# Optimization experiments

Hardware: AMD Instinct MI355X
Metric: run time of the kernel (lower is better)

The kernel has to match this reference:

```python
import jax, jax.numpy as jnp
import numpy as np

B, S, DIM = 2, 2048, 2048
H = 16
Q_RANK, KV_RANK = 512, 512
D_NOPE, D_ROPE, D_V = 128, 64, 128
D_QK = D_NOPE + D_ROPE  # 192
EPS = 1e-6
SCALE = D_QK ** -0.5


def setup_inputs() -> dict:
    key = jax.random.key(0)
    ks = jax.random.split(key, 8)
    x = jax.random.normal(ks[0], (B, S, DIM), dtype=jnp.float32)
    # real RoPE table: theta_i = 10000^{-2i/d}, angles = pos * theta
    inv_freq = 1.0 / (10000.0 ** (np.arange(0, D_ROPE, 2, dtype=np.float32) / D_ROPE))
    ang = np.arange(S, dtype=np.float32)[:, None] * inv_freq[None, :]  # (S, D_ROPE//2)
    freqs_cis = jnp.asarray(np.stack([np.cos(ang), np.sin(ang)], axis=-1))  # (S, 32, 2)
    std = 0.02
    wq_a = jax.random.normal(ks[1], (Q_RANK, DIM), dtype=jnp.float32) * std
    wq_b = jax.random.normal(ks[2], (H * D_QK, Q_RANK), dtype=jnp.float32) * std
    wkv_a = jax.random.normal(ks[3], (KV_RANK + D_ROPE, DIM), dtype=jnp.float32) * std
    wkv_b = jax.random.normal(ks[4], (H * (D_NOPE + D_V), KV_RANK), dtype=jnp.float32) * std
    wo = jax.random.normal(ks[5], (DIM, H * D_V), dtype=jnp.float32) * std
    q_norm_w = jnp.ones((Q_RANK,), dtype=jnp.float32)
    kv_norm_w = jnp.ones((KV_RANK,), dtype=jnp.float32)
    return {"x": x, "freqs_cis": freqs_cis, "wq_a": wq_a, "wq_b": wq_b,
            "q_norm_w": q_norm_w, "wkv_a": wkv_a, "kv_norm_w": kv_norm_w,
            "wkv_b": wkv_b, "wo": wo}


def _rmsnorm(x, w):
    var = jnp.mean(jnp.square(x), axis=-1, keepdims=True)
    return x * jax.lax.rsqrt(var + EPS) * w


def _rope(x, freqs_cis):
    # x: (B, S, h, d); freqs_cis: (S, d//2, 2) as (cos, sin). Pairs are interleaved (x0,x1),(x2,x3),...
    xr, xi = x[..., 0::2], x[..., 1::2]
    cos = freqs_cis[None, :, None, :, 0]
    sin = freqs_cis[None, :, None, :, 1]
    yr = xr * cos - xi * sin
    yi = xr * sin + xi * cos
    return jnp.stack([yr, yi], axis=-1).reshape(x.shape)


def reference(x, freqs_cis, wq_a, wq_b, q_norm_w, wkv_a, kv_norm_w, wkv_b, wo):
    b, s, _ = x.shape
    # low-rank Q projection: wq_a -> RMSNorm -> wq_b
    q = _rmsnorm(x @ wq_a.T, q_norm_w) @ wq_b.T
    q = q.reshape(b, s, H, D_QK)
    q_nope, q_pe = q[..., :D_NOPE], q[..., D_NOPE:]
    q = jnp.concatenate([q_nope, _rope(q_pe, freqs_cis)], axis=-1)  # (b,s,H,192)
    # KV path
    kv = x @ wkv_a.T  # (b,s,KV_RANK+D_ROPE)
    kv_lat, k_pe = kv[..., :KV_RANK], kv[..., KV_RANK:]
    k_pe = _rope(k_pe[:, :, None, :], freqs_cis)  # (b,s,1,64)
    kv = (_rmsnorm(kv_lat, kv_norm_w) @ wkv_b.T).reshape(b, s, H, D_NOPE + D_V)
    k_nope, v = kv[..., :D_NOPE], kv[..., D_NOPE:]
    k = jnp.concatenate([k_nope, jnp.broadcast_to(k_pe, (b, s, H, D_ROPE))], axis=-1)
    # causal scaled-dot-product attention
    scores = jnp.einsum('bshd,bthd->bhst', q, k) * SCALE
    mask = jnp.tril(jnp.ones((s, s), dtype=bool))
    scores = jnp.where(mask[None, None], scores, jnp.finfo(scores.dtype).min)
    probs = jax.nn.softmax(scores, axis=-1)
    out = jnp.einsum('bhst,bthd->bshd', probs, v).reshape(b, s, H * D_V)
    return out @ wo.T
```

## Files before the change

### kernel.cpp

```cpp
#include <hip/hip_runtime.h>
#include <cstdint>
#include <cstddef>


typedef unsigned short u16;
typedef unsigned int u32;
typedef unsigned long long u64;
typedef __attribute__((ext_vector_type(8))) short bf16x8;
typedef __attribute__((ext_vector_type(4))) float floatx4;

#define MFMA16x16x32 __builtin_amdgcn_mfma_f32_16x16x32_bf16

#define QSCALE 0.10411755f
#define THR_L2 11.541560f

__device__ __forceinline__ u16 f2bf(float f) {
  u32 u = __float_as_uint(f);
  u32 r = (u + 0x7fffu + ((u >> 16) & 1u)) >> 16;
  return (u16)r;
}
__device__ __forceinline__ float bf2f(u16 b) {
  return __uint_as_float(((u32)b) << 16);
}
__device__ __forceinline__ u32 cvtpk(float lo, float hi) {
  u32 r;
  asm("v_cvt_pk_bf16_f32 %0, %1, %2" : "=v"(r) : "v"(lo), "v"(hi));
  return r;
}
__device__ __forceinline__ void gload16(const void* g, void* l) {
  __builtin_amdgcn_global_load_lds(
      (const __attribute__((address_space(1))) void*)g,
      (__attribute__((address_space(3))) void*)l, 16, 0, 0);
}

__global__ __launch_bounds__(256) void cvt_all(
    const float* __restrict__ s0, const float* __restrict__ s1,
    const float* __restrict__ s2, const float* __restrict__ s3,
    const float* __restrict__ s4, const float* __restrict__ s5,
    u16* __restrict__ d0, u16* __restrict__ d1, u16* __restrict__ d2,
    u16* __restrict__ d3, u16* __restrict__ d4, u16* __restrict__ d5) {
  constexpr int ST1 = 2097152;
  constexpr int ST2 = ST1 + 262144;
  constexpr int ST3 = ST2 + 294912;
  constexpr int ST4 = ST3 + 393216;
  constexpr int ST5 = ST4 + 524288;
  constexpr int TOT = ST5 + 1048576;
  int i = blockIdx.x * 256 + threadIdx.x;
  int stride = gridDim.x * 256;
  for (; i < TOT; i += stride) {
    const float* sp;
    u16* dp;
    int j;
    if (i < ST1)      { sp = s0; dp = d0; j = i; }
    else if (i < ST2) { sp = s1; dp = d1; j = i - ST1; }
    else if (i < ST3) { sp = s2; dp = d2; j = i - ST2; }
    else if (i < ST4) { sp = s3; dp = d3; j = i - ST3; }
    else if (i < ST5) { sp = s4; dp = d4; j = i - ST4; }
    else              { sp = s5; dp = d5; j = i - ST5; }
    float4 v = ((const float4*)sp)[j];
    ushort4 o;
    o.x = f2bf(v.x); o.y = f2bf(v.y); o.z = f2bf(v.z); o.w = f2bf(v.w);
    ((ushort4*)dp)[j] = o;
  }
}

template <int BM, int BN, int EPI>
__global__ __launch_bounds__(512) void gemm8(const u16* __restrict__ A,
                                             const u16* __restrict__ B,
                                             void* __restrict__ Cv,
                                             int M, int N, int K,
                                             const float* __restrict__ fcp,
                                             void* __restrict__ aux) {
  constexpr int WM = BM / 2;
  constexpr int AF = WM / 16;
  constexpr int WN = BN / 4;
  constexpr int FN = WN / 16;
  constexpr int LA = BM * 4 / 512;
  constexpr int LB = BN * 4 / 512;
  constexpr int S = LA + LB;
  __shared__ alignas(16) u16 As[2][BM * 32];
  __shared__ alignas(16) u16 Bs[2][BN * 32];
  const int m0 = blockIdx.y * BM, n0 = blockIdx.x * BN;
  const int t = threadIdx.x;
  const int wv = t >> 6, lane = t & 63, g = lane >> 4, qq = lane & 15;
  const int wr = wv >> 2, wc = wv & 3;
  const int fsw = (qq >> 1) & 3;
  size_t aoff[LA], boff[LB];
#pragma unroll
  for (int i = 0; i < LA; ++i) {
    int seg = t + i * 512;
    int row = seg >> 2, sl = seg & 3;
    aoff[i] = (size_t)(m0 + row) * K + (sl ^ ((row >> 1) & 3)) * 8;
  }
#pragma unroll
  for (int i = 0; i < LB; ++i) {
    int seg = t + i * 512;
    int row = seg >> 2, sl = seg & 3;
    boff[i] = (size_t)(n0 + row) * K + (sl ^ ((row >> 1) & 3)) * 8;
  }
  const floatx4 fz = {0.f, 0.f, 0.f, 0.f};
  floatx4 acc[AF][FN];
#pragma unroll
  for (int m = 0; m < AF; ++m)
#pragma unroll
    for (int n = 0; n < FN; ++n) acc[m][n] = fz;

#define GS8(buf, k0)                                                          \
  {                                                                           \
    _Pragma("unroll") for (int i = 0; i < LA; ++i)                            \
        gload16(&A[aoff[i] + (k0)], &As[buf][(size_t)(wv * 64 + i * 512) * 8]); \
    _Pragma("unroll") for (int i = 0; i < LB; ++i)                            \
        gload16(&B[boff[i] + (k0)], &Bs[buf][(size_t)(wv * 64 + i * 512) * 8]); \
  }

  const int nk = K >> 5;
  GS8(0, 0);
  GS8(1, 32);
  for (int kt = 0; kt < nk; ++kt) {
    asm volatile("" ::: "memory");
    if (kt + 1 < nk) {
      if constexpr (S == 4)
        asm volatile("s_waitcnt vmcnt(4)" ::: "memory");
      else if constexpr (S == 3)
        asm volatile("s_waitcnt vmcnt(3)" ::: "memory");
      else
        asm volatile("s_waitcnt vmcnt(2)" ::: "memory");
    } else {
      asm volatile("s_waitcnt vmcnt(0)" ::: "memory");
    }
    __builtin_amdgcn_s_barrier();
    asm volatile("" ::: "memory");
    const u16* Ab = &As[kt & 1][0];
    const u16* Bb = &Bs[kt & 1][0];
    bf16x8 af[AF], bfr[FN];
#pragma unroll
    for (int m = 0; m < AF; ++m)
      af[m] = *(const bf16x8*)&Ab[(wr * WM + m * 16 + qq) * 32 + ((g ^ fsw) * 8)];
#pragma unroll
    for (int n = 0; n < FN; ++n)
      bfr[n] = *(const bf16x8*)&Bb[(wc * WN + n * 16 + qq) * 32 + ((g ^ fsw) * 8)];
    asm volatile("s_waitcnt lgkmcnt(0)" ::: "memory");
    __builtin_amdgcn_s_barrier();
    asm volatile("" ::: "memory");
    if (kt + 2 < nk) GS8(kt & 1, (kt + 2) * 32);
    __builtin_amdgcn_s_setprio(1);
#pragma unroll
    for (int m = 0; m < AF; ++m)
#pragma unroll
      for (int n = 0; n < FN; ++n)
        acc[m][n] = MFMA16x16x32(af[m], bfr[n], acc[m][n], 0, 0, 0);
    __builtin_amdgcn_s_setprio(0);
  }
#undef GS8

#pragma unroll
  for (int m = 0; m < AF; ++m)
#pragma unroll
    for (int n = 0; n < FN; ++n) {
      const int col16 = n0 + wc * WN + n * 16;
      if constexpr (EPI == 0 || EPI == 1) {
#pragma unroll
        for (int r = 0; r < 4; ++r) {
          int row = m0 + wr * WM + m * 16 + 4 * g + r;
          int col = col16 + qq;
          if constexpr (EPI == 1)
            ((u16*)Cv)[(size_t)row * N + col] = f2bf(acc[m][n][r]);
          else
            ((float*)Cv)[(size_t)row * N + col] = acc[m][n][r];
        }
      } else if constexpr (EPI == 2) {
        const int h = col16 / 192;
        const int jb = col16 - h * 192 + qq;
#pragma unroll
        for (int r = 0; r < 4; ++r) {
          int row = m0 + wr * WM + m * 16 + 4 * g + r;
          int b = row >> 11, s = row & 2047;
          float own = acc[m][n][r];
          float par = __shfl_xor(own, 1);
          if ((qq & 1) == 0) {
            u32 w;
            if (jb < 128) {
              w = cvtpk(own * QSCALE, par * QSCALE);
            } else {
              int jp = (jb - 128) >> 1;
              float c = fcp[(s * 32 + jp) * 2];
              float sn = fcp[(s * 32 + jp) * 2 + 1];
              w = cvtpk((own * c - par * sn) * QSCALE,
                        (own * sn + par * c) * QSCALE);
            }
            *(u32*)((u16*)Cv + ((size_t)(b * 16 + h) * 2048 + s) * 192 + jb) = w;
          }
        }
      } else {
        const int h = col16 >> 8;
        const int jb = (col16 & 255) + qq;
        if (jb < 128) {
#pragma unroll
          for (int r = 0; r < 4; ++r) {
            int row = m0 + wr * WM + m * 16 + 4 * g + r;
            int b = row >> 11, s = row & 2047;
            float own = acc[m][n][r];
            float par = __shfl_xor(own, 1);
            if ((qq & 1) == 0)
              *(u32*)((u16*)Cv + ((size_t)(b * 16 + h) * 2048 + s) * 192 + jb) =
                  cvtpk(own, par);
          }
        } else {
          int row0 = m0 + wr * WM + m * 16 + 4 * g;
          int b = row0 >> 11, s0v = row0 & 2047;
          int dv = jb - 128;
          u32 lo = cvtpk(acc[m][n][0], acc[m][n][1]);
          u32 hi = cvtpk(acc[m][n][2], acc[m][n][3]);
          u64 w = (u64)lo | ((u64)hi << 32);
          *(u64*)((u16*)aux + ((size_t)(b * 16 + h) * 128 + dv) * 2048 + s0v) = w;
        }
      }
    }
}

__global__ __launch_bounds__(256) void rmsnorm_u16(const u16* __restrict__ in,
                                                   int stride,
                                                   const float* __restrict__ w,
                                                   u16* __restrict__ out) {
  const int row = blockIdx.x, t = threadIdx.x;
  __shared__ float wsum[4];
  u32 wv2 = *(const u32*)&in[(size_t)row * stride + 2 * t];
  float vx = bf2f((u16)wv2), vy = bf2f((u16)(wv2 >> 16));
  float ss = vx * vx + vy * vy;
#pragma unroll
  for (int off = 1; off < 64; off <<= 1) ss += __shfl_xor(ss, off);
  if ((t & 63) == 0) wsum[t >> 6] = ss;
  __syncthreads();
  float tot = wsum[0] + wsum[1] + wsum[2] + wsum[3];
  float r = rsqrtf(tot * (1.f / 512.f) + 1e-6f);
  *(u32*)&out[(size_t)row * 512 + 2 * t] =
      cvtpk(vx * r * w[2 * t], vy * r * w[2 * t + 1]);
}

__global__ __launch_bounds__(256) void rope_kpe_bcast(const u16* __restrict__ ap,
                                                      const float* __restrict__ fc,
                                                      u16* __restrict__ kbf) {
  int idx = blockIdx.x * 256 + threadIdx.x;
  int row = idx >> 5, j = idx & 31;
  int b = row >> 11, s = row & 2047;
  u32 wv2 = *(const u32*)&ap[(size_t)row * 1280 + 1024 + 2 * j];
  float xr = bf2f((u16)wv2), xi = bf2f((u16)(wv2 >> 16));
  float c = fc[(s * 32 + j) * 2], sn = fc[(s * 32 + j) * 2 + 1];
  u32 w = cvtpk(xr * c - xi * sn, xr * sn + xi * c);
#pragma unroll
  for (int h = 0; h < 16; ++h)
    *(u32*)&kbf[((size_t)(b * 16 + h) * 2048 + s) * 192 + 128 + 2 * j] = w;
}

__global__ __launch_bounds__(256, 4) void flash_attn(const u16* __restrict__ Q,
                                                     const u16* __restrict__ Kc,
                                                     const u16* __restrict__ VT,
                                                     u16* __restrict__ O) {
  __shared__ alignas(16) u16 Ks[2][32 * 192];
  __shared__ alignas(16) u16 Vs[2][128 * 32];
  const int QT[32] = {31, 30, 29, 28, 27, 26, 25, 24, 0,  1,  2,  3,  4,  5,
                      6,  7,  23, 22, 21, 20, 19, 18, 17, 16, 8,  9,  10, 11,
                      12, 13, 14, 15};
  const int bid = blockIdx.x;
  const int qt = QT[bid >> 5];
  const int bh = bid & 31;
  const int t = threadIdx.x, wv = t >> 6, lane = t & 63;
  const int g = lane >> 4, qq = lane & 15;
  const int qrow0 = qt * 64 + wv * 16;
  const int my_last = qrow0 + 15;
  const int q_glob = qrow0 + qq;
  const int nkt = 2 * qt + 2;

  int koffg[3], voffg[2];
#pragma unroll
  for (int i = 0; i < 3; ++i) {
    int seg = t + i * 256;
    int row = seg / 24, sl = seg - row * 24;
    koffg[i] = row * 192 + (sl ^ ((row >> 1) & 7)) * 8;
  }
#pragma unroll
  for (int i = 0; i < 2; ++i) {
    int seg = t + i * 256;
    int row = seg >> 2, sl = seg & 3;
    voffg[i] = row * 2048 + (sl ^ ((row >> 1) & 3)) * 8;
  }
  const u16* Kt0 = Kc + (size_t)bh * 2048 * 192;
  const u16* Vt0 = VT + (size_t)bh * 128 * 2048;

  bf16x8 qf[6];
  {
    const u16* qp = Q + ((size_t)bh * 2048 + qrow0 + qq) * 192;
#pragma unroll
    for (int kk = 0; kk < 6; ++kk) qf[kk] = *(const bf16x8*)&qp[kk * 32 + g * 8];
  }
  asm volatile("s_waitcnt vmcnt(0)" ::: "memory");

  const floatx4 fz = {0.f, 0.f, 0.f, 0.f};
  floatx4 oacc[8];
  floatx4 oacc_l = fz;
#pragma unroll
  for (int d = 0; d < 8; ++d) oacc[d] = fz;
  float m_run = -1e30f;

  bf16x8 ones;
#pragma unroll
  for (int i = 0; i < 8; ++i) ones[i] = (short)0x3f80;

  const int krow0 = 2 * qq;
  const int krow1 = 2 * qq + 1;
  const int xrk = qq & 7;
  const int vsw = (qq >> 1) & 3;

#define STAGE(buf, kt)                                                       \
  {                                                                          \
    const u16* Kg = Kt0 + (size_t)(kt) * (32 * 192);                         \
    const u16* Vg = Vt0 + (kt) * 32;                                         \
    _Pragma("unroll") for (int i = 0; i < 3; ++i)                            \
        gload16(Kg + koffg[i], &Ks[buf][(size_t)(wv * 64 + i * 256) * 8]);   \
    _Pragma("unroll") for (int i = 0; i < 2; ++i)                            \
        gload16(Vg + voffg[i], &Vs[buf][(size_t)(wv * 64 + i * 256) * 8]);   \
  }

  STAGE(0, 0);
  for (int kt = 0; kt < nkt; ++kt) {
    const int k0 = kt * 32;
    asm volatile("" ::: "memory");
    if (kt + 1 < nkt) {
      STAGE((kt + 1) & 1, kt + 1);
      asm volatile("s_waitcnt vmcnt(5)" ::: "memory");
    } else {
      asm volatile("s_waitcnt vmcnt(0)" ::: "memory");
    }
    __builtin_amdgcn_s_barrier();
    asm volatile("" ::: "memory");
    if (k0 <= my_last) {
      const u16* Kb = &Ks[kt & 1][0];
      const u16* Vb = &Vs[kt & 1][0];
      floatx4 s0 = fz, s1 = fz;
      __builtin_amdgcn_s_setprio(1);
#pragma unroll
      for (int kk = 0; kk < 6; ++kk) {
        int sl = kk * 4 + g;
        bf16x8 a0 = *(const bf16x8*)&Kb[krow0 * 192 + ((sl ^ xrk) * 8)];
        bf16x8 a1 = *(const bf16x8*)&Kb[krow1 * 192 + ((sl ^ xrk) * 8)];
        s0 = MFMA16x16x32(a0, qf[kk], s0, 0, 0, 0);
        s1 = MFMA16x16x32(a1, qf[kk], s1, 0, 0, 0);
      }
      __builtin_amdgcn_s_setprio(0);
      float v[8];
      if (k0 + 31 <= qrow0) {
#pragma unroll
        for (int r = 0; r < 4; ++r) {
          v[r] = s0[r];
          v[4 + r] = s1[r];
        }
      } else {
#pragma unroll
        for (int r = 0; r < 4; ++r) {
          int key0 = k0 + 8 * g + 2 * r;
          v[r] = (key0 <= q_glob) ? s0[r] : -1e30f;
          v[4 + r] = (key0 + 1 <= q_glob) ? s1[r] : -1e30f;
        }
      }
      float mloc = fmaxf(fmaxf(fmaxf(v[0], v[1]), fmaxf(v[2], v[3])),
                         fmaxf(fmaxf(v[4], v[5]), fmaxf(v[6], v[7])));
      if (!__all(mloc <= m_run + THR_L2)) {
        float mx = fmaxf(mloc, __shfl_xor(mloc, 16));
        mx = fmaxf(mx, __shfl_xor(mx, 32));
        float m_new = fmaxf(m_run, mx);
        float alpha = exp2f(m_run - m_new);
        m_run = m_new;
#pragma unroll
        for (int d = 0; d < 8; ++d)
#pragma unroll
          for (int r = 0; r < 4; ++r) oacc[d][r] *= alpha;
#pragma unroll
        for (int r = 0; r < 4; ++r) oacc_l[r] *= alpha;
      }
      float pex[8];
#pragma unroll
      for (int i = 0; i < 8; ++i) pex[i] = exp2f(v[i] - m_run);
      bf16x8 pf;
      ((u32*)&pf)[0] = cvtpk(pex[0], pex[4]);
      ((u32*)&pf)[1] = cvtpk(pex[1], pex[5]);
      ((u32*)&pf)[2] = cvtpk(pex[2], pex[6]);
      ((u32*)&pf)[3] = cvtpk(pex[3], pex[7]);
      __builtin_amdgcn_s_setprio(1);
#pragma unroll
      for (int d = 0; d < 8; ++d) {
        bf16x8 vf = *(const bf16x8*)&Vb[(d * 16 + qq) * 32 + ((g ^ vsw) * 8)];
        oacc[d] = MFMA16x16x32(vf, pf, oacc[d], 0, 0, 0);
      }
      oacc_l = MFMA16x16x32(ones, pf, oacc_l, 0, 0, 0);
      __builtin_amdgcn_s_setprio(0);
    }
    asm volatile("" ::: "memory");
    __builtin_amdgcn_s_barrier();
  }
#undef STAGE
  float linv = 1.f / oacc_l[0];
  const int b = bh >> 4, h = bh & 15;
  size_t rowoff = ((size_t)b * 2048 + qrow0 + qq) * 2048 + h * 128 + 4 * g;
#pragma unroll
  for (int d = 0; d < 8; ++d) {
    u32 lo = cvtpk(oacc[d][0] * linv, oacc[d][1] * linv);
    u32 hi = cvtpk(oacc[d][2] * linv, oacc[d][3] * linv);
    u64 w = (u64)lo | ((u64)hi << 32);
    *(u64*)&O[rowoff + d * 16] = w;
  }
}

extern "C" void kernel_launch(void* const* d_in, const int* in_sizes, int n_in,
                              void* d_out, int out_size, void* d_ws,
                              size_t ws_size, hipStream_t stream) {
  (void)in_sizes; (void)n_in; (void)out_size;
  const float* x = (const float*)d_in[0];
  const float* fc = (const float*)d_in[1];
  const float* wqa = (const float*)d_in[2];
  const float* wqb = (const float*)d_in[3];
  const float* qnw = (const float*)d_in[4];
  const float* wkva = (const float*)d_in[5];
  const float* kvnw = (const float*)d_in[6];
  const float* wkvb = (const float*)d_in[7];
  const float* wo = (const float*)d_in[8];
  float* out = (float*)d_out;
  char* ws = (char*)d_ws;

  size_t off = 0;
  auto alloc = [&](size_t bytes) {
    size_t o = off;
    off += (bytes + 255) & ~(size_t)255;
    return o;
  };
  const size_t o_xbf = alloc(16777216);
  const size_t o_wa = alloc(5242880);
  const size_t o_wqb = alloc(3145728);
  const size_t o_wkvb = alloc(4194304);
  const size_t o_wo = alloc(8388608);
  const size_t o_qln = alloc(4194304);
  const size_t o_kvln = alloc(4194304);
  const size_t o_ap = alloc(10485760);
  const size_t o_qbf = alloc(25165824);
  const size_t o_kbf = alloc(25165824);
  const size_t o_vt = alloc(16777216);
  if (ws_size < off) return;

  u16* xbf = (u16*)(ws + o_xbf);
  u16* wab = (u16*)(ws + o_wa);
  u16* wqbb = (u16*)(ws + o_wqb);
  u16* wkvbb = (u16*)(ws + o_wkvb);
  u16* wob = (u16*)(ws + o_wo);
  u16* qlatn = (u16*)(ws + o_qln);
  u16* kvlatn = (u16*)(ws + o_kvln);
  u16* ap = (u16*)(ws + o_ap);
  u16* qbf = (u16*)(ws + o_qbf);
  u16* kbf = (u16*)(ws + o_kbf);
  u16* vt = (u16*)(ws + o_vt);
  u16* attnbf = (u16*)(ws + o_xbf);

  cvt_all<<<2048, 256, 0, stream>>>(x, wqa, wkva, wqb, wkvb, wo,
                                    xbf, wab, wab + 1048576, wqbb, wkvbb, wob);

  gemm8<128, 128, 1><<<dim3(10, 32), 512, 0, stream>>>(
      xbf, wab, ap, 4096, 1280, 2048, nullptr, nullptr);
  rmsnorm_u16<<<4096, 256, 0, stream>>>(ap, 1280, qnw, qlatn);
  rmsnorm_u16<<<4096, 256, 0, stream>>>(ap + 512, 1280, kvnw, kvlatn);
  rope_kpe_bcast<<<512, 256, 0, stream>>>(ap, fc, kbf);

  gemm8<128, 256, 2><<<dim3(12, 32), 512, 0, stream>>>(
      qlatn, wqbb, qbf, 4096, 3072, 512, fc, nullptr);

  gemm8<128, 256, 3><<<dim3(16, 32), 512, 0, stream>>>(
      kvlatn, wkvbb, kbf, 4096, 4096, 512, nullptr, vt);

  flash_attn<<<1024, 256, 0, stream>>>(qbf, kbf, vt, attnbf);
  gemm8<128, 128, 0><<<dim3(16, 32), 512, 0, stream>>>(
      attnbf, wob, out, 4096, 2048, 2048, nullptr, nullptr);
}
```

Before: 248.5 us.

## Use 128-row query tiles with 8 waves in flash attention and fuse RMSNorm launches

Flash attention now uses 512-thread blocks covering 128 query rows, so each K/V tile staged into shared memory serves twice as many waves. The grid is halved and the staging and wait counts are rearranged to match. This cuts redundant global K/V traffic, at the cost of coarser causal load balance and fewer blocks in flight. The two RMSNorm launches are also merged into one kernel to save a launch.

```diff
diff --git a/kernel.cpp b/kernel.cpp
--- a/kernel.cpp
+++ b/kernel.cpp
@@ -218,13 +218,19 @@
     }
 }
 
-__global__ __launch_bounds__(256) void rmsnorm_u16(const u16* __restrict__ in,
-                                                   int stride,
-                                                   const float* __restrict__ w,
-                                                   u16* __restrict__ out) {
-  const int row = blockIdx.x, t = threadIdx.x;
+__global__ __launch_bounds__(256) void rmsnorm2(const u16* __restrict__ ap,
+                                                const float* __restrict__ qw,
+                                                const float* __restrict__ kw,
+                                                u16* __restrict__ qout,
+                                                u16* __restrict__ kout) {
+  const int bid = blockIdx.x, t = threadIdx.x;
+  const bool isq = bid < 4096;
+  const int row = isq ? bid : bid - 4096;
+  const u16* in = ap + (size_t)row * 1280 + (isq ? 0 : 512);
+  const float* w = isq ? qw : kw;
+  u16* out = (isq ? qout : kout) + (size_t)row * 512;
   __shared__ float wsum[4];
-  u32 wv2 = *(const u32*)&in[(size_t)row * stride + 2 * t];
+  u32 wv2 = *(const u32*)&in[2 * t];
   float vx = bf2f((u16)wv2), vy = bf2f((u16)(wv2 >> 16));
   float ss = vx * vx + vy * vy;
 #pragma unroll
@@ -233,8 +239,7 @@
   __syncthreads();
   float tot = wsum[0] + wsum[1] + wsum[2] + wsum[3];
   float r = rsqrtf(tot * (1.f / 512.f) + 1e-6f);
-  *(u32*)&out[(size_t)row * 512 + 2 * t] =
-      cvtpk(vx * r * w[2 * t], vy * r * w[2 * t + 1]);
+  *(u32*)&out[2 * t] = cvtpk(vx * r * w[2 * t], vy * r * w[2 * t + 1]);
 }
 
 __global__ __launch_bounds__(256) void rope_kpe_bcast(const u16* __restrict__ ap,
@@ -252,37 +257,32 @@
     *(u32*)&kbf[((size_t)(b * 16 + h) * 2048 + s) * 192 + 128 + 2 * j] = w;
 }
 
-__global__ __launch_bounds__(256, 4) void flash_attn(const u16* __restrict__ Q,
+__global__ __launch_bounds__(512, 4) void flash_attn(const u16* __restrict__ Q,
                                                      const u16* __restrict__ Kc,
                                                      const u16* __restrict__ VT,
                                                      u16* __restrict__ O) {
   __shared__ alignas(16) u16 Ks[2][32 * 192];
   __shared__ alignas(16) u16 Vs[2][128 * 32];
-  const int QT[32] = {31, 30, 29, 28, 27, 26, 25, 24, 0,  1,  2,  3,  4,  5,
-                      6,  7,  23, 22, 21, 20, 19, 18, 17, 16, 8,  9,  10, 11,
-                      12, 13, 14, 15};
+  const int QT16[16] = {15, 14, 13, 12, 11, 10, 9, 8, 0, 1, 2, 3, 4, 5, 6, 7};
   const int bid = blockIdx.x;
-  const int qt = QT[bid >> 5];
+  const int qt = QT16[bid >> 5];
   const int bh = bid & 31;
   const int t = threadIdx.x, wv = t >> 6, lane = t & 63;
   const int g = lane >> 4, qq = lane & 15;
-  const int qrow0 = qt * 64 + wv * 16;
+  const int qrow0 = qt * 128 + wv * 16;
   const int my_last = qrow0 + 15;
   const int q_glob = qrow0 + qq;
-  const int nkt = 2 * qt + 2;
-
-  int koffg[3], voffg[2];
-#pragma unroll
-  for (int i = 0; i < 3; ++i) {
-    int seg = t + i * 256;
-    int row = seg / 24, sl = seg - row * 24;
-    koffg[i] = row * 192 + (sl ^ ((row >> 1) & 7)) * 8;
-  }
-#pragma unroll
-  for (int i = 0; i < 2; ++i) {
-    int seg = t + i * 256;
-    int row = seg >> 2, sl = seg & 3;
-    voffg[i] = row * 2048 + (sl ^ ((row >> 1) & 3)) * 8;
+  const int nkt = 4 * qt + 4;
+
+  int koffg0, koffg1, voffg0;
+  {
+    int row = t / 24, sl = t - row * 24;
+    koffg0 = row * 192 + (sl ^ ((row >> 1) & 7)) * 8;
+    int seg = t + 512;
+    row = seg / 24; sl = seg - row * 24;
+    koffg1 = row * 192 + (sl ^ ((row >> 1) & 7)) * 8;
+    row = t >> 2; sl = t & 3;
+    voffg0 = row * 2048 + (sl ^ ((row >> 1) & 3)) * 8;
   }
   const u16* Kt0 = Kc + (size_t)bh * 2048 * 192;
   const u16* Vt0 = VT + (size_t)bh * 128 * 2048;
@@ -311,14 +311,13 @@
   const int xrk = qq & 7;
   const int vsw = (qq >> 1) & 3;
 
-#define STAGE(buf, kt)                                                       \
-  {                                                                          \
-    const u16* Kg = Kt0 + (size_t)(kt) * (32 * 192);                         \
-    const u16* Vg = Vt0 + (kt) * 32;                                         \
-    _Pragma("unroll") for (int i = 0; i < 3; ++i)                            \
-        gload16(Kg + koffg[i], &Ks[buf][(size_t)(wv * 64 + i * 256) * 8]);   \
-    _Pragma("unroll") for (int i = 0; i < 2; ++i)                            \
-        gload16(Vg + voffg[i], &Vs[buf][(size_t)(wv * 64 + i * 256) * 8]);   \
+#define STAGE(buf, kt)                                                        \
+  {                                                                           \
+    const u16* Kg = Kt0 + (size_t)(kt) * (32 * 192);                          \
+    const u16* Vg = Vt0 + (kt) * 32;                                          \
+    gload16(Kg + koffg0, &Ks[buf][(size_t)(wv * 64) * 8]);                    \
+    if (wv < 4) gload16(Kg + koffg1, &Ks[buf][(size_t)(512 + wv * 64) * 8]);  \
+    gload16(Vg + voffg0, &Vs[buf][(size_t)(wv * 64) * 8]);                    \
   }
 
   STAGE(0, 0);
@@ -327,7 +326,10 @@
     asm volatile("" ::: "memory");
     if (kt + 1 < nkt) {
       STAGE((kt + 1) & 1, kt + 1);
-      asm volatile("s_waitcnt vmcnt(5)" ::: "memory");
+      if (wv < 4)
+        asm volatile("s_waitcnt vmcnt(3)" ::: "memory");
+      else
+        asm volatile("s_waitcnt vmcnt(2)" ::: "memory");
     } else {
       asm volatile("s_waitcnt vmcnt(0)" ::: "memory");
     }
@@ -463,8 +465,7 @@
 
   gemm8<128, 128, 1><<<dim3(10, 32), 512, 0, stream>>>(
       xbf, wab, ap, 4096, 1280, 2048, nullptr, nullptr);
-  rmsnorm_u16<<<4096, 256, 0, stream>>>(ap, 1280, qnw, qlatn);
-  rmsnorm_u16<<<4096, 256, 0, stream>>>(ap + 512, 1280, kvnw, kvlatn);
+  rmsnorm2<<<8192, 256, 0, stream>>>(ap, qnw, kvnw, qlatn, kvlatn);
   rope_kpe_bcast<<<512, 256, 0, stream>>>(ap, fc, kbf);
 
   gemm8<128, 256, 2><<<dim3(12, 32), 512, 0, stream>>>(
@@ -473,7 +474,7 @@
   gemm8<128, 256, 3><<<dim3(16, 32), 512, 0, stream>>>(
       kvlatn, wkvbb, kbf, 4096, 4096, 512, nullptr, vt);
 
-  flash_attn<<<1024, 256, 0, stream>>>(qbf, kbf, vt, attnbf);
+  flash_attn<<<512, 512, 0, stream>>>(qbf, kbf, vt, attnbf);
   gemm8<128, 128, 0><<<dim3(16, 32), 512, 0, stream>>>(
       attnbf, wob, out, 4096, 2048, 2048, nullptr, nullptr);
 }
```

After: 253.6 us. 2.0% more time.
